# Kernel optimization log

Measured on AMD Instinct MI355X. Metric: run time of the kernel, lower is better.

The kernel has to match this reference:

```python
import jax, jax.numpy as jnp
import numpy as np

# ---- Build Cayley tables for projective GA G(3,0,1), basis ordered by grade ----
_BLADES = [(), (0,), (1,), (2,), (3,), (0,1), (0,2), (0,3), (1,2), (1,3), (2,3),
           (0,1,2), (0,1,3), (0,2,3), (1,2,3), (0,1,2,3)]
_IDX = {b: i for i, b in enumerate(_BLADES)}

def _blade_mul(a, b, metric):
    """Multiply basis blades a*b. Returns (sign, result_blade); sign=0 if it vanishes."""
    arr = list(a) + list(b)
    sign = 1
    changed = True
    while changed:
        changed = False
        for i in range(len(arr) - 1):
            if arr[i] > arr[i + 1]:
                arr[i], arr[i + 1] = arr[i + 1], arr[i]
                sign = -sign
                changed = True
            elif arr[i] == arr[i + 1]:
                sign *= metric[arr[i]]
                del arr[i:i + 2]
                changed = True
                break
    return sign, tuple(arr)

def _build_tables():
    metric = [0, 1, 1, 1]  # e0^2 = 0 (degenerate), e1^2=e2^2=e3^2=1
    G = np.zeros((16, 16, 16), np.float32)  # geometric product
    W = np.zeros((16, 16, 16), np.float32)  # outer (wedge) product
    for a in _BLADES:
        for b in _BLADES:
            s, r = _blade_mul(a, b, metric)
            if s != 0:
                G[_IDX[a], _IDX[b], _IDX[r]] = s
            if not (set(a) & set(b)):
                s2, r2 = _blade_mul(a, b, [1, 1, 1, 1])
                W[_IDX[a], _IDX[b], _IDX[r2]] = s2
    # Right-complement dual: dual(e_a) = s * e_c with e_a ^ dual(e_a) = e0123
    full = (0, 1, 2, 3)
    dual_idx = np.zeros(16, np.int32)
    dual_sign = np.zeros(16, np.float32)
    for a in _BLADES:
        c = tuple(sorted(set(full) - set(a)))
        s, _ = _blade_mul(a, c, [1, 1, 1, 1])
        dual_idx[_IDX[a]] = _IDX[c]
        dual_sign[_IDX[a]] = s
    # Coefficient map: dual(x)[j] = dual_sign[dual_idx[j]] * x[dual_idx[j]]
    out_sign = dual_sign[dual_idx]
    return jnp.asarray(G), jnp.asarray(W), jnp.asarray(dual_idx), jnp.asarray(out_sign)

_G, _W, _DUAL_IDX, _DUAL_SIGN = _build_tables()
_PSS = 15  # index of pseudoscalar e0123

def _dual(x):
    return x[..., _DUAL_IDX] * _DUAL_SIGN


def setup_inputs() -> dict:
    key = jax.random.key(0)
    k1, k2, k3 = jax.random.split(key, 3)
    B, T, C = 64, 8192, 16
    return {
        "x": jax.random.normal(k1, (B, T, C), dtype=jnp.float32),
        "y": jax.random.normal(k2, (B, T, C), dtype=jnp.float32),
        "ref": jax.random.normal(k3, (B, T, C), dtype=jnp.float32),
    }


def reference(x, y, ref):
    # Geometric product over the Cayley table
    gp = jnp.einsum("bti,btj,ijk->btk", x, y, _G)
    # E(3)-equivariant join: ref_e0123 * dual(dual(x) ^ dual(y))
    wedge = jnp.einsum("bti,btj,ijk->btk", _dual(x), _dual(y), _W)
    join = ref[..., _PSS:_PSS + 1] * _dual(wedge)
    return jnp.concatenate([gp, join], axis=-1)  # (B, T, 32)
```

## Files before the change

kernel.cpp:

```cpp
#include <hip/hip_runtime.h>

namespace ga {

constexpr int MASK[16]        = {0,1,2,4,8,3,5,9,6,10,12,7,11,13,14,15};
constexpr int IDX_OF_MASK[16] = {0,1,2,5,3,6,8,11,4,7,9,12,10,13,14,15};

constexpr int popc(int v) { int c = 0; while (v) { c += v & 1; v >>= 1; } return c; }

constexpr int reorder_sign(int a, int b) {
    int s = 0; int t = a >> 1;
    while (t) { s += popc(t & b); t >>= 1; }
    return (s & 1) ? -1 : 1;
}

struct Term { signed char i, j, k, s; };

struct GPTab { Term t[192]; };
constexpr GPTab build_gp() {
    GPTab T{}; int n = 0;
    for (int i = 0; i < 16; i++)
        for (int j = 0; j < 16; j++) {
            int a = MASK[i], b = MASK[j];
            if (a & b & 1) continue;
            T.t[n].i = (signed char)i;
            T.t[n].j = (signed char)j;
            T.t[n].k = (signed char)IDX_OF_MASK[a ^ b];
            T.t[n].s = (signed char)reorder_sign(a, b);
            n++;
        }
    return T;
}

struct JNTab { Term t[81]; };
constexpr JNTab build_join() {
    JNTab T{}; int n = 0;
    int didx[16] = {}, dsgn[16] = {};
    for (int i = 0; i < 16; i++) {
        int a = MASK[i], c = (~a) & 0xF;
        didx[i] = IDX_OF_MASK[c];
        dsgn[i] = reorder_sign(a, c);
    }
    for (int i = 0; i < 16; i++)
        for (int j = 0; j < 16; j++) {
            int p = didx[i], q = didx[j];
            int a = MASK[p], b = MASK[q];
            if (a & b) continue;
            int m = IDX_OF_MASK[a | b];
            int k = didx[m];
            int s = dsgn[i] * dsgn[j] * dsgn[m] * reorder_sign(a, b);
            T.t[n].i = (signed char)i;
            T.t[n].j = (signed char)j;
            T.t[n].k = (signed char)k;
            T.t[n].s = (signed char)s;
            n++;
        }
    return T;
}

constexpr GPTab G = build_gp();
constexpr JNTab J = build_join();

}


typedef const __attribute__((address_space(1))) void* gas_ptr;
typedef __attribute__((address_space(3))) void*       las_ptr;

constexpr int NITER = 4;

__global__ __launch_bounds__(64, 2)
void MVGeometricBilinear_kernel(const float* __restrict__ x,
                                const float* __restrict__ y,
                                const float* __restrict__ ref,
                                float* __restrict__ out,
                                int nchunks, int gstride)
{
    __shared__ __align__(16) float buf[2][2048];

    const int lane = threadIdx.x;
    const long chunk0 = blockIdx.x;
    if (chunk0 >= nchunks) return;

    float rr[NITER];
    {
        long c = chunk0;
#pragma unroll
        for (int it = 0; it < NITER; ++it) {
            if (c < nchunks) rr[it] = ref[(c * 64 + lane) * 16 + 15];
            c += gstride;
        }
    }

    int srcoff[4];
    int fragoff[4];
#pragma unroll
    for (int k = 0; k < 4; ++k) {
        const int slot = k * 64 + lane;
        const int j = ((slot & 3) - ((slot >> 3) & 3)) & 3;
        srcoff[k] = (slot & ~3) | j;
        const int s = (k + ((lane >> 1) & 3)) & 3;
        fragoff[k] = lane * 16 + (s << 2);
    }

    const float4* gx = reinterpret_cast<const float4*>(x);
    const float4* gy = reinterpret_cast<const float4*>(y);

    auto dma = [&](long c, int b) {
#pragma unroll
        for (int k = 0; k < 4; ++k)
            __builtin_amdgcn_global_load_lds((gas_ptr)(gx + c * 256 + srcoff[k]),
                                             (las_ptr)(&buf[b][k * 256]), 16, 0, 0);
#pragma unroll
        for (int k = 0; k < 4; ++k)
            __builtin_amdgcn_global_load_lds((gas_ptr)(gy + c * 256 + srcoff[k]),
                                             (las_ptr)(&buf[b][1024 + k * 256]), 16, 0, 0);
    };

    long chunk = chunk0;
    int cur = 0;
    dma(chunk, 0);

#pragma unroll
    for (int it = 0; it < NITER; ++it) {
        const long next = chunk + gstride;
        const bool pf = (it + 1 < NITER) && (next < nchunks);
        if (pf) dma(next, cur ^ 1);

        if (it == 0) {
            if (pf) asm volatile("s_waitcnt vmcnt(8)" ::: "memory");
            else    asm volatile("s_waitcnt vmcnt(0)" ::: "memory");
        } else {
            if (pf) asm volatile("s_waitcnt vmcnt(16)" ::: "memory");
            else    asm volatile("s_waitcnt vmcnt(8)" ::: "memory");
        }

        float xx[16], yy[16];
#pragma unroll
        for (int k = 0; k < 4; ++k) {
            const float4 vx = *reinterpret_cast<const float4*>(&buf[cur][fragoff[k]]);
            const float4 vy = *reinterpret_cast<const float4*>(&buf[cur][1024 + fragoff[k]]);
            xx[4*k+0] = vx.x; xx[4*k+1] = vx.y; xx[4*k+2] = vx.z; xx[4*k+3] = vx.w;
            yy[4*k+0] = vy.x; yy[4*k+1] = vy.y; yy[4*k+2] = vy.z; yy[4*k+3] = vy.w;
        }
        const float r = rr[it];

        float gp[16] = {0.f,0.f,0.f,0.f,0.f,0.f,0.f,0.f,
                        0.f,0.f,0.f,0.f,0.f,0.f,0.f,0.f};
        float jn[16] = {0.f,0.f,0.f,0.f,0.f,0.f,0.f,0.f,
                        0.f,0.f,0.f,0.f,0.f,0.f,0.f,0.f};
#pragma unroll
        for (int t = 0; t < 192; t++) {
            const int ti = ga::G.t[t].i, tj = ga::G.t[t].j, tk = ga::G.t[t].k;
            const float v = xx[ti] * yy[tj];
            if (ga::G.t[t].s > 0) gp[tk] += v; else gp[tk] -= v;
        }
#pragma unroll
        for (int t = 0; t < 81; t++) {
            const int ti = ga::J.t[t].i, tj = ga::J.t[t].j, tk = ga::J.t[t].k;
            const float v = xx[ti] * yy[tj];
            if (ga::J.t[t].s > 0) jn[tk] += v; else jn[tk] -= v;
        }

        asm volatile("" ::: "memory");

        float* lo = &buf[cur][0];
        const int px = lane & 7;
#pragma unroll
        for (int q = 0; q < 4; q++)
            *reinterpret_cast<float4*>(lo + lane * 32 + ((q ^ px) << 2)) =
                make_float4(gp[4*q+0], gp[4*q+1], gp[4*q+2], gp[4*q+3]);
#pragma unroll
        for (int q = 0; q < 4; q++)
            *reinterpret_cast<float4*>(lo + lane * 32 + (((q + 4) ^ px) << 2)) =
                make_float4(r*jn[4*q+0], r*jn[4*q+1], r*jn[4*q+2], r*jn[4*q+3]);

        asm volatile("s_waitcnt lgkmcnt(0)" ::: "memory");

        float4* go = reinterpret_cast<float4*>(out) + chunk * 512;
#pragma unroll
        for (int c = 0; c < 8; c++) {
            const int g = c * 64 + lane;
            const int p = g >> 3, q = g & 7;
            go[g] = *reinterpret_cast<const float4*>(
                        lo + p * 32 + ((q ^ (p & 7)) << 2));
        }

        asm volatile("" ::: "memory");

        if (!pf) break;
        cur ^= 1;
        chunk = next;
    }
}

__global__ __launch_bounds__(64)
void MVGeometricBilinear_tail(const float* __restrict__ x,
                              const float* __restrict__ y,
                              const float* __restrict__ ref,
                              float* __restrict__ out,
                              int start, int npts)
{
    int pt = start + blockIdx.x * 64 + threadIdx.x;
    if (pt >= npts) return;
    float xx[16], yy[16];
#pragma unroll
    for (int k = 0; k < 16; k++) { xx[k] = x[(size_t)pt*16+k]; yy[k] = y[(size_t)pt*16+k]; }
    const float r = ref[(size_t)pt*16+15];
    float gp[16] = {}, jn[16] = {};
#pragma unroll
    for (int t = 0; t < 192; t++) {
        const float v = xx[ga::G.t[t].i] * yy[ga::G.t[t].j];
        if (ga::G.t[t].s > 0) gp[ga::G.t[t].k] += v; else gp[ga::G.t[t].k] -= v;
    }
#pragma unroll
    for (int t = 0; t < 81; t++) {
        const float v = xx[ga::J.t[t].i] * yy[ga::J.t[t].j];
        if (ga::J.t[t].s > 0) jn[ga::J.t[t].k] += v; else jn[ga::J.t[t].k] -= v;
    }
#pragma unroll
    for (int k = 0; k < 16; k++) out[(size_t)pt*32+k] = gp[k];
#pragma unroll
    for (int k = 0; k < 16; k++) out[(size_t)pt*32+16+k] = r * jn[k];
}

extern "C" void kernel_launch(void* const* d_in, const int* in_sizes, int n_in,
                              void* d_out, int out_size, void* d_ws, size_t ws_size,
                              hipStream_t stream) {
    const float* x   = (const float*)d_in[0];
    const float* y   = (const float*)d_in[1];
    const float* ref = (const float*)d_in[2];
    float* out = (float*)d_out;

    const int npts    = in_sizes[0] / 16;
    const int nchunks = npts / 64;

    if (nchunks > 0) {
        int blocks = nchunks < 2560 ? nchunks : 2560;
        const int need = (nchunks + NITER - 1) / NITER;
        if (blocks < need) blocks = need;
        MVGeometricBilinear_kernel<<<blocks, 64, 0, stream>>>(
            x, y, ref, out, nchunks, blocks);
    }

    const int rem = npts - nchunks * 64;
    if (rem > 0) {
        MVGeometricBilinear_tail<<<(rem + 63) / 64, 64, 0, stream>>>(
            x, y, ref, out, nchunks * 64, npts);
    }
}
```

Baseline: 147.2 us.

## Replace LDS DMA double buffer with register prefetch and single LDS buffer

```diff
diff --git a/kernel.cpp b/kernel.cpp
--- a/kernel.cpp
+++ b/kernel.cpp
@@ -63,19 +63,16 @@
 }
 
 
-typedef const __attribute__((address_space(1))) void* gas_ptr;
-typedef __attribute__((address_space(3))) void*       las_ptr;
-
 constexpr int NITER = 4;
 
-__global__ __launch_bounds__(64, 2)
+__global__ __launch_bounds__(64, 4)
 void MVGeometricBilinear_kernel(const float* __restrict__ x,
                                 const float* __restrict__ y,
                                 const float* __restrict__ ref,
                                 float* __restrict__ out,
                                 int nchunks, int gstride)
 {
-    __shared__ __align__(16) float buf[2][2048];
+    __shared__ __align__(16) float buf[2048];
 
     const int lane = threadIdx.x;
     const long chunk0 = blockIdx.x;
@@ -91,54 +88,52 @@
         }
     }
 
-    int srcoff[4];
-    int fragoff[4];
+    int wslot[4], fragoff[4];
 #pragma unroll
     for (int k = 0; k < 4; ++k) {
-        const int slot = k * 64 + lane;
-        const int j = ((slot & 3) - ((slot >> 3) & 3)) & 3;
-        srcoff[k] = (slot & ~3) | j;
-        const int s = (k + ((lane >> 1) & 3)) & 3;
-        fragoff[k] = lane * 16 + (s << 2);
+        const int g = k * 64 + lane;
+        const int p = g >> 2;
+        const int s = (p << 2) | (((g & 3) + ((p >> 1) & 3)) & 3);
+        wslot[k] = s << 2;
+        fragoff[k] = (lane << 4) + (((k + ((lane >> 1) & 3)) & 3) << 2);
     }
 
     const float4* gx = reinterpret_cast<const float4*>(x);
     const float4* gy = reinterpret_cast<const float4*>(y);
 
-    auto dma = [&](long c, int b) {
+    float4 P[8];
+    auto prefetch = [&](long c) {
+#pragma unroll
+        for (int k = 0; k < 4; ++k) P[k]     = gx[c * 256 + k * 64 + lane];
+#pragma unroll
+        for (int k = 0; k < 4; ++k) P[4 + k] = gy[c * 256 + k * 64 + lane];
+    };
+    auto commit = [&]() {
 #pragma unroll
         for (int k = 0; k < 4; ++k)
-            __builtin_amdgcn_global_load_lds((gas_ptr)(gx + c * 256 + srcoff[k]),
-                                             (las_ptr)(&buf[b][k * 256]), 16, 0, 0);
+            *reinterpret_cast<float4*>(&buf[wslot[k]]) = P[k];
 #pragma unroll
         for (int k = 0; k < 4; ++k)
-            __builtin_amdgcn_global_load_lds((gas_ptr)(gy + c * 256 + srcoff[k]),
-                                             (las_ptr)(&buf[b][1024 + k * 256]), 16, 0, 0);
+            *reinterpret_cast<float4*>(&buf[1024 + wslot[k]]) = P[4 + k];
     };
 
+    prefetch(chunk0);
+    asm volatile("s_waitcnt vmcnt(0)" ::: "memory");
+    commit();
+    asm volatile("" ::: "memory");
+
     long chunk = chunk0;
-    int cur = 0;
-    dma(chunk, 0);
-
 #pragma unroll
     for (int it = 0; it < NITER; ++it) {
         const long next = chunk + gstride;
         const bool pf = (it + 1 < NITER) && (next < nchunks);
-        if (pf) dma(next, cur ^ 1);
-
-        if (it == 0) {
-            if (pf) asm volatile("s_waitcnt vmcnt(8)" ::: "memory");
-            else    asm volatile("s_waitcnt vmcnt(0)" ::: "memory");
-        } else {
-            if (pf) asm volatile("s_waitcnt vmcnt(16)" ::: "memory");
-            else    asm volatile("s_waitcnt vmcnt(8)" ::: "memory");
-        }
+        if (pf) prefetch(next);
 
         float xx[16], yy[16];
 #pragma unroll
         for (int k = 0; k < 4; ++k) {
-            const float4 vx = *reinterpret_cast<const float4*>(&buf[cur][fragoff[k]]);
-            const float4 vy = *reinterpret_cast<const float4*>(&buf[cur][1024 + fragoff[k]]);
+            const float4 vx = *reinterpret_cast<const float4*>(&buf[fragoff[k]]);
+            const float4 vy = *reinterpret_cast<const float4*>(&buf[1024 + fragoff[k]]);
             xx[4*k+0] = vx.x; xx[4*k+1] = vx.y; xx[4*k+2] = vx.z; xx[4*k+3] = vx.w;
             yy[4*k+0] = vy.x; yy[4*k+1] = vy.y; yy[4*k+2] = vy.z; yy[4*k+3] = vy.w;
         }
@@ -163,32 +158,35 @@
 
         asm volatile("" ::: "memory");
 
-        float* lo = &buf[cur][0];
         const int px = lane & 7;
 #pragma unroll
         for (int q = 0; q < 4; q++)
-            *reinterpret_cast<float4*>(lo + lane * 32 + ((q ^ px) << 2)) =
+            *reinterpret_cast<float4*>(&buf[lane * 32 + ((q ^ px) << 2)]) =
                 make_float4(gp[4*q+0], gp[4*q+1], gp[4*q+2], gp[4*q+3]);
 #pragma unroll
         for (int q = 0; q < 4; q++)
-            *reinterpret_cast<float4*>(lo + lane * 32 + (((q + 4) ^ px) << 2)) =
+            *reinterpret_cast<float4*>(&buf[lane * 32 + (((q + 4) ^ px) << 2)]) =
                 make_float4(r*jn[4*q+0], r*jn[4*q+1], r*jn[4*q+2], r*jn[4*q+3]);
 
         asm volatile("s_waitcnt lgkmcnt(0)" ::: "memory");
 
-        float4* go = reinterpret_cast<float4*>(out) + chunk * 512;
-#pragma unroll
-        for (int c = 0; c < 8; c++) {
-            const int g = c * 64 + lane;
-            const int p = g >> 3, q = g & 7;
-            go[g] = *reinterpret_cast<const float4*>(
-                        lo + p * 32 + ((q ^ (p & 7)) << 2));
-        }
-
+        {
+            float4* go = reinterpret_cast<float4*>(out) + chunk * 512;
+#pragma unroll
+            for (int c = 0; c < 8; c++) {
+                const int g = c * 64 + lane;
+                const int p = g >> 3, q = g & 7;
+                go[g] = *reinterpret_cast<const float4*>(
+                            &buf[p * 32 + ((q ^ (p & 7)) << 2)]);
+            }
+        }
         asm volatile("" ::: "memory");
 
         if (!pf) break;
-        cur ^= 1;
+
+        asm volatile("s_waitcnt vmcnt(8)" ::: "memory");
+        commit();
+        asm volatile("" ::: "memory");
         chunk = next;
     }
 }
@@ -235,7 +233,7 @@
     const int nchunks = npts / 64;
 
     if (nchunks > 0) {
-        int blocks = nchunks < 2560 ? nchunks : 2560;
+        int blocks = nchunks < 2048 ? nchunks : 2048;
         const int need = (nchunks + NITER - 1) / NITER;
         if (blocks < need) blocks = need;
         MVGeometricBilinear_kernel<<<blocks, 64, 0, stream>>>(
```

Result: slower. 164.8 us (+12.0%).
